# Kernel tuning notes

Measured on AMD Instinct MI355X. Metric: run time of the kernel, lower is better.

Reference implementation:

```python
import jax, jax.numpy as jnp
import numpy as np

HEADS = 8
DIM_HEAD = 64


def setup_inputs() -> dict:
    key = jax.random.key(0)
    ks = jax.random.split(key, 5)
    dim = 512
    dim_inner = HEADS * DIM_HEAD
    return {
        "fmap": jax.random.normal(ks[0], (8, dim, 32, 32), dtype=jnp.float32),
        "gamma": jnp.ones((dim,), dtype=jnp.float32),
        "wq": jax.random.normal(ks[1], (dim_inner, dim), dtype=jnp.float32) * 0.05,
        "wv": jax.random.normal(ks[2], (dim_inner, dim), dtype=jnp.float32) * 0.05,
        "null_kv": jax.random.normal(ks[3], (2, HEADS, DIM_HEAD), dtype=jnp.float32),
        "wo": jax.random.normal(ks[4], (dim, dim_inner), dtype=jnp.float32) * 0.05,
    }


def reference(fmap, gamma, wq, wv, null_kv, wo):
    b, c, H, W = fmap.shape
    h, d = HEADS, DIM_HEAD
    n = H * W
    scale = d ** (-0.5)

    # ChannelRMSNorm: F.normalize over channel dim * sqrt(dim) * gamma
    l2 = jnp.sqrt(jnp.sum(fmap * fmap, axis=1, keepdims=True))
    x = fmap / jnp.maximum(l2, 1e-12) * (c ** 0.5) * gamma[None, :, None, None]

    # 1x1 convs as channel matmuls -> [b, h, n, d]
    def proj(w):
        t = jnp.einsum('bcxy,oc->boxy', x, w)          # [b, h*d, H, W]
        return t.reshape(b, h, d, n).transpose(0, 1, 3, 2)  # [b, h, n, d]

    q = proj(wq)
    v = proj(wv)
    k = q  # dot_product=False -> to_k is None, k = q

    # prepend null kv token
    nk = jnp.broadcast_to(null_kv[0][None, :, None, :], (b, h, 1, d))
    nv = jnp.broadcast_to(null_kv[1][None, :, None, :], (b, h, 1, d))
    k = jnp.concatenate([nk, k], axis=2)  # [b, h, n+1, d]
    v = jnp.concatenate([nv, v], axis=2)

    # negative squared L2 distance score: -(|q|^2 + |k|^2 - 2 q.k)
    q_sq = jnp.sum(q * q, axis=-1)  # [b, h, n]
    k_sq = jnp.sum(k * k, axis=-1)  # [b, h, n+1]
    qk = jnp.einsum('bhid,bhjd->bhij', q, k)
    sim = -(q_sq[..., :, None] + k_sq[..., None, :] - 2.0 * qk) * scale

    attn = jax.nn.softmax(sim, axis=-1)
    out = jnp.einsum('bhij,bhjd->bhid', attn, v)  # [b, h, n, d]

    out = out.transpose(0, 1, 3, 2).reshape(b, h * d, H, W)
    return jnp.einsum('boxy,co->bcxy', out, wo)
```

## Files before the change

kernel.cpp:

```cpp
#include <hip/hip_runtime.h>
#include <hip/hip_bf16.h>

#define DEV static __device__ __forceinline__

typedef __bf16 bf16x8 __attribute__((ext_vector_type(8)));
typedef float f32x4 __attribute__((ext_vector_type(4)));
typedef float f32x16 __attribute__((ext_vector_type(16)));
typedef unsigned u32x4 __attribute__((ext_vector_type(4)));
typedef unsigned short u16x8 __attribute__((ext_vector_type(8)));
typedef unsigned short u16x4 __attribute__((ext_vector_type(4)));

DEV unsigned short f2bf(float f) {
  unsigned u = __builtin_bit_cast(unsigned, f);
  u += 0x7fffu + ((u >> 16) & 1u);
  return (unsigned short)(u >> 16);
}
DEV float bf2f(unsigned short s) {
  return __builtin_bit_cast(float, (unsigned)s << 16);
}
DEV f32x4 mfma16(bf16x8 a, bf16x8 b, f32x4 c) {
  return __builtin_amdgcn_mfma_f32_16x16x32_bf16(a, b, c, 0, 0, 0);
}
DEV f32x16 mfma32(bf16x8 a, bf16x8 b, f32x16 c) {
  return __builtin_amdgcn_mfma_f32_32x32x16_bf16(a, b, c, 0, 0, 0);
}
DEV bf16x8 ld8(const unsigned short* p) {
  return __builtin_bit_cast(bf16x8, *(const u16x8*)p);
}
DEV void gload16(const unsigned short* g, unsigned short* l) {
  auto* g1 = reinterpret_cast<const __attribute__((address_space(1))) unsigned int*>(
      reinterpret_cast<uintptr_t>(g));
  auto* l3 = reinterpret_cast<__attribute__((address_space(3))) unsigned int*>(
      reinterpret_cast<uintptr_t>(l));
  __builtin_amdgcn_global_load_lds(g1, l3, 16, 0, 0);
}

__global__ __launch_bounds__(256) void prep_k(const float* __restrict__ fmap,
                                              const float* __restrict__ gamma,
                                              const float* __restrict__ wq,
                                              const float* __restrict__ wv,
                                              const float* __restrict__ wo,
                                              unsigned short* __restrict__ xt,
                                              unsigned short* __restrict__ wqb,
                                              unsigned short* __restrict__ wvb,
                                              unsigned short* __restrict__ wob) {
  int bid = blockIdx.x, tid = threadIdx.x;
  if (bid >= 256) {
    int t4 = bid - 256;
    int g = t4 >> 5;
    const float* src = (g == 0) ? wq : (g == 1) ? wv : wo;
    unsigned short* dst = (g == 0) ? wqb : (g == 1) ? wvb : wob;
    int base = (t4 & 31) * 1024 + tid;
    const float4* s = (const float4*)src;
#pragma unroll
    for (int i = 0; i < 4; ++i) {
      int idx = base + i * 256;
      float4 a = s[idx * 2], b = s[idx * 2 + 1];
      u16x8 o;
      o[0] = f2bf(a.x); o[1] = f2bf(a.y); o[2] = f2bf(a.z); o[3] = f2bf(a.w);
      o[4] = f2bf(b.x); o[5] = f2bf(b.y); o[6] = f2bf(b.z); o[7] = f2bf(b.w);
      ((u16x8*)dst)[idx] = o;
    }
    return;
  }
  __shared__ float red[8][32];
  __shared__ float rn_l[32];
  __shared__ float gl[512];
  __shared__ float t[64][33];
  int b = bid >> 5, n0 = (bid & 31) * 32;
  gl[tid] = gamma[tid];
  gl[tid + 256] = gamma[tid + 256];
  int n_l = tid & 31, cg = tid >> 5;
  const float* p = fmap + ((size_t)(b * 512 + cg * 64)) * 1024 + n0 + n_l;
  float s = 0.f;
#pragma unroll 16
  for (int i = 0; i < 64; ++i) { float v = p[i * 1024]; s += v * v; }
  red[cg][n_l] = s;
  __syncthreads();
  if (tid < 32) {
    float ts = 0.f;
#pragma unroll
    for (int k = 0; k < 8; ++k) ts += red[k][tid];
    rn_l[tid] = 22.62741699796952f / fmaxf(sqrtf(ts), 1e-12f);
  }
  __syncthreads();
  int nn = tid >> 3, cc = tid & 7;
  for (int c0 = 0; c0 < 512; c0 += 64) {
#pragma unroll
    for (int i = 0; i < 8; ++i)
      t[cg * 8 + i][n_l] = fmap[((size_t)(b * 512 + c0 + cg * 8 + i)) * 1024 + n0 + n_l];
    __syncthreads();
    float sc = rn_l[nn];
    u16x8 o;
#pragma unroll
    for (int e = 0; e < 8; ++e) o[e] = f2bf(t[cc * 8 + e][nn] * sc * gl[c0 + cc * 8 + e]);
    *(u16x8*)(xt + ((size_t)(b * 1024 + n0 + nn)) * 512 + c0 + cc * 8) = o;
    __syncthreads();
  }
}

__global__ __launch_bounds__(256) void gemm_qv_k(const unsigned short* __restrict__ A,
                                                 const unsigned short* __restrict__ wqb,
                                                 const unsigned short* __restrict__ wvb,
                                                 const float* __restrict__ nkv,
                                                 unsigned short* __restrict__ QF,
                                                 unsigned short* __restrict__ VF,
                                                 float* __restrict__ qsqs,
                                                 float* __restrict__ p0g) {
  __shared__ unsigned short a_lds[128 * 64];
  __shared__ unsigned short b_lds[128 * 64];
  const unsigned short* Bt = blockIdx.z ? wvb : wqb;
  int tid = threadIdx.x, lane = tid & 63, wid = tid >> 6;
  int wr = wid >> 1, wc = wid & 1;
  int m0 = blockIdx.y * 128, n0 = blockIdx.x * 128;
  int srow = (lane >> 3);
  int scol = ((lane & 7) ^ ((lane >> 3) & 7)) * 8;
  f32x4 acc[4][4] = {};
  for (int kt = 0; kt < 512; kt += 64) {
#pragma unroll
    for (int i = 0; i < 4; ++i) {
      int il = wid * 4 + i;
      gload16(A + (size_t)(m0 + il * 8 + srow) * 512 + kt + scol, &a_lds[il * 512]);
      gload16(Bt + (size_t)(n0 + il * 8 + srow) * 512 + kt + scol, &b_lds[il * 512]);
    }
    __syncthreads();
#pragma unroll
    for (int ks = 0; ks < 2; ++ks) {
      int c = ks * 4 + (lane >> 4);
      int cs = (c ^ (lane & 7)) * 8;
      bf16x8 af[4], bfr[4];
#pragma unroll
      for (int rt = 0; rt < 4; ++rt)
        af[rt] = ld8(&a_lds[(wr * 64 + rt * 16 + (lane & 15)) * 64 + cs]);
#pragma unroll
      for (int ct = 0; ct < 4; ++ct)
        bfr[ct] = ld8(&b_lds[(wc * 64 + ct * 16 + (lane & 15)) * 64 + cs]);
#pragma unroll
      for (int rt = 0; rt < 4; ++rt)
#pragma unroll
        for (int ct = 0; ct < 4; ++ct)
          acc[rt][ct] = mfma16(af[rt], bfr[ct], acc[rt][ct]);
    }
    __syncthreads();
  }
  if (blockIdx.z == 0) {
    const float COEF = 0.18033688011112042f;
    int head = blockIdx.x * 2 + wc;
    const float* nk = nkv + head * 64;
    float nk_own[4], nks = 0.f;
#pragma unroll
    for (int ct = 0; ct < 4; ++ct) {
      nk_own[ct] = nk[ct * 16 + (lane & 15)];
      nks += nk_own[ct] * nk_own[ct];
    }
    nks += __shfl_xor(nks, 1); nks += __shfl_xor(nks, 2);
    nks += __shfl_xor(nks, 4); nks += __shfl_xor(nks, 8);
#pragma unroll
    for (int rt = 0; rt < 4; ++rt)
#pragma unroll
      for (int r = 0; r < 4; ++r) {
        float qs = 0.f, dot = 0.f;
        unsigned short qr[4];
#pragma unroll
        for (int ct = 0; ct < 4; ++ct) {
          unsigned short us = f2bf(acc[rt][ct][r]);
          qr[ct] = us;
          float v = bf2f(us);
          qs += v * v;
          dot += v * nk_own[ct];
        }
        int n = m0 + wr * 64 + rt * 16 + (lane >> 4) * 4 + r;
        int bb = n >> 10, nl = n & 1023;
        int bh = bb * 8 + head;
        size_t fidx = (size_t)(bh * 32 + (nl >> 5)) * 2048 + (nl & 31) * 16 + (lane & 15);
#pragma unroll
        for (int ct = 0; ct < 4; ++ct) QF[fidx + ct * 512] = qr[ct];
        qs += __shfl_xor(qs, 1); qs += __shfl_xor(qs, 2);
        qs += __shfl_xor(qs, 4); qs += __shfl_xor(qs, 8);
        dot += __shfl_xor(dot, 1); dot += __shfl_xor(dot, 2);
        dot += __shfl_xor(dot, 4); dot += __shfl_xor(dot, 8);
        if ((lane & 15) == 0) {
          qsqs[bh * 1024 + nl] = qs * COEF;
          p0g[bh * 1024 + nl] = __builtin_amdgcn_exp2f((2.f * dot - nks) * COEF);
        }
      }
  } else {
#pragma unroll
    for (int rt = 0; rt < 4; ++rt)
#pragma unroll
      for (int ct = 0; ct < 4; ++ct) {
        int nb = m0 + wr * 64 + rt * 16 + (lane >> 4) * 4;
        int o = n0 + wc * 64 + ct * 16 + (lane & 15);
        int b = nb >> 10, j = nb & 1023;
        int h = o >> 6, d = o & 63;
        int bh = b * 8 + h;
        size_t idx = (size_t)(bh * 32 + (j >> 5)) * 2048 + ((j >> 4) & 1) * 1024 + (d >> 5) * 512 +
                     (d & 31) * 16 + (j & 15);
        u16x4 pk;
#pragma unroll
        for (int r = 0; r < 4; ++r) pk[r] = f2bf(acc[rt][ct][r]);
        *(u16x4*)(VF + idx) = pk;
      }
  }
}

__global__ __launch_bounds__(256) void gemm_o_k(const unsigned short* __restrict__ A,
                                                const unsigned short* __restrict__ Bt,
                                                float* __restrict__ Cp) {
  __shared__ unsigned short a_lds[64 * 64];
  __shared__ unsigned short b_lds[128 * 64];
  int bid = blockIdx.x;
  int y = (bid >> 3) & 7;
  int x = (bid & 7) + ((bid >> 6) << 3);
  int m0 = y * 64, n0 = x * 128;
  int tid = threadIdx.x, lane = tid & 63, wid = tid >> 6;
  int wr = wid >> 1, wc = wid & 1;
  int srow = (lane >> 3);
  int scol = ((lane & 7) ^ ((lane >> 3) & 7)) * 8;
  f32x4 acc[2][4] = {};
  for (int kt = 0; kt < 512; kt += 64) {
#pragma unroll
    for (int i = 0; i < 2; ++i) {
      int il = wid * 2 + i;
      gload16(A + (size_t)(m0 + il * 8 + srow) * 512 + kt + scol, &a_lds[il * 512]);
    }
#pragma unroll
    for (int i = 0; i < 4; ++i) {
      int il = wid * 4 + i;
      gload16(Bt + (size_t)(n0 + il * 8 + srow) * 512 + kt + scol, &b_lds[il * 512]);
    }
    __syncthreads();
#pragma unroll
    for (int ks = 0; ks < 2; ++ks) {
      int c = ks * 4 + (lane >> 4);
      int cs = (c ^ (lane & 7)) * 8;
      bf16x8 af[2], bfr[4];
#pragma unroll
      for (int rt = 0; rt < 2; ++rt)
        af[rt] = ld8(&a_lds[(wr * 32 + rt * 16 + (lane & 15)) * 64 + cs]);
#pragma unroll
      for (int ct = 0; ct < 4; ++ct)
        bfr[ct] = ld8(&b_lds[(wc * 64 + ct * 16 + (lane & 15)) * 64 + cs]);
#pragma unroll
      for (int rt = 0; rt < 2; ++rt)
#pragma unroll
        for (int ct = 0; ct < 4; ++ct)
          acc[rt][ct] = mfma16(af[rt], bfr[ct], acc[rt][ct]);
    }
    __syncthreads();
  }
  int bb = n0 >> 10;
#pragma unroll
  for (int rt = 0; rt < 2; ++rt)
#pragma unroll
    for (int ct = 0; ct < 4; ++ct)
#pragma unroll
      for (int r = 0; r < 4; ++r) {
        int row = m0 + wr * 32 + rt * 16 + (lane >> 4) * 4 + r;
        int col = (n0 & 1023) + wc * 64 + ct * 16 + (lane & 15);
        Cp[((size_t)(bb * 512 + row)) * 1024 + col] = acc[rt][ct][r];
      }
}

__global__ __launch_bounds__(512) void attn_k(const unsigned short* __restrict__ QF,
                                              const unsigned short* __restrict__ VF,
                                              const float* __restrict__ qsqs,
                                              const float* __restrict__ p0g,
                                              const float* __restrict__ nkv,
                                              unsigned short* __restrict__ att) {
  const float C2 = 0.36067376022224085f;
  int bid = blockIdx.x;
  int s0 = bid >> 3;
  int bh = ((bid & 7) << 3) | (s0 & 7);
  int qt = s0 >> 3;
  int b = bh >> 3, h = bh & 7;
  int n0 = qt * 128;
  int tid = threadIdx.x, lane = tid & 63, wid = tid >> 6;
  int wq = wid & 3, jg = wid >> 2;
  int l31 = lane & 31, hi = lane >> 5;

  __shared__ float ob_l[32][4][64];
  __shared__ float dsb[4][32];
  __shared__ float p0_l[128];
  __shared__ float nv_l[64];
  __shared__ float dn_l[4][32];

  if (tid < 128) p0_l[tid] = p0g[bh * 1024 + n0 + tid];
  else if (tid < 192) nv_l[tid - 128] = nkv[512 + h * 64 + (tid - 128)];
  __syncthreads();

  bf16x8 qf[4];
  const unsigned short* qfp = QF + (size_t)(bh * 32 + qt * 4 + wq) * 2048 + l31 * 16 + hi * 8;
#pragma unroll
  for (int ks = 0; ks < 4; ++ks)
    qf[ks] = ld8(qfp + ks * 512);

  f32x16 oacc[2];
#pragma unroll
  for (int dh = 0; dh < 2; ++dh)
#pragma unroll
    for (int r = 0; r < 16; ++r) {
      int row = (r & 3) + 8 * (r >> 2) + 4 * hi;
      oacc[dh][r] = (jg == 0) ? p0_l[wq * 32 + row] * nv_l[dh * 32 + l31] : 0.f;
    }

  f32x4 dsum4 = {0.f, 0.f, 0.f, 0.f};
  const unsigned short* kbase = QF + (size_t)bh * 65536 + l31 * 16 + hi * 8;
  const unsigned short* vbase = VF + (size_t)bh * 65536 + l31 * 16 + hi * 8;
  const float* ksb = qsqs + bh * 1024 + 4 * hi;

  bf16x8 kfA[4], kfB[4], vfA[2][2], vfB[2][2];
  f32x4 ksqA[4], ksqB[4];

#define LOADT(S, JT)                                                        \
  {                                                                         \
    const unsigned short* kp_ = kbase + (JT) * 2048;                        \
    kf##S[0] = ld8(kp_);        kf##S[1] = ld8(kp_ + 512);                  \
    kf##S[2] = ld8(kp_ + 1024); kf##S[3] = ld8(kp_ + 1536);                 \
    const unsigned short* vp_ = vbase + (JT) * 2048;                        \
    vf##S[0][0] = ld8(vp_);        vf##S[0][1] = ld8(vp_ + 1024);           \
    vf##S[1][0] = ld8(vp_ + 512);  vf##S[1][1] = ld8(vp_ + 1536);           \
    const float* kq_ = ksb + (JT) * 32;                                     \
    ksq##S[0] = *(const f32x4*)(kq_);      ksq##S[1] = *(const f32x4*)(kq_ + 8);  \
    ksq##S[2] = *(const f32x4*)(kq_ + 16); ksq##S[3] = *(const f32x4*)(kq_ + 24); \
  }

#define COMPT(S)                                                            \
  {                                                                         \
    f32x16 sacc = {};                                                       \
    __builtin_amdgcn_s_setprio(1);                                          \
    sacc = mfma32(kf##S[0], qf[0], sacc);                                   \
    sacc = mfma32(kf##S[1], qf[1], sacc);                                   \
    sacc = mfma32(kf##S[2], qf[2], sacc);                                   \
    sacc = mfma32(kf##S[3], qf[3], sacc);                                   \
    __builtin_amdgcn_s_setprio(0);                                          \
    float p[16];                                                            \
    _Pragma("unroll")                                                       \
    for (int r = 0; r < 16; ++r) {                                          \
      p[r] = __builtin_amdgcn_exp2f(sacc[r] * C2 - ksq##S[r >> 2][r & 3]);  \
      dsum4[r & 3] += p[r];                                                 \
    }                                                                       \
    unsigned w[4][2];                                                       \
    _Pragma("unroll")                                                       \
    for (int m = 0; m < 4; ++m) {                                           \
      asm("v_cvt_pk_bf16_f32 %0, %1, %2" : "=v"(w[m][0]) : "v"(p[4 * m]), "v"(p[4 * m + 1]));     \
      asm("v_cvt_pk_bf16_f32 %0, %1, %2" : "=v"(w[m][1]) : "v"(p[4 * m + 2]), "v"(p[4 * m + 3])); \
    }                                                                       \
    __builtin_amdgcn_s_setprio(1);                                          \
    _Pragma("unroll")                                                       \
    for (int sj = 0; sj < 2; ++sj) {                                        \
      unsigned a0 = w[2 * sj][0], b0 = w[2 * sj + 1][0];                    \
      unsigned a1 = w[2 * sj][1], b1 = w[2 * sj + 1][1];                    \
      asm("v_permlane32_swap_b32 %0, %1" : "+v"(a0), "+v"(b0));             \
      asm("v_permlane32_swap_b32 %0, %1" : "+v"(a1), "+v"(b1));             \
      u32x4 pw; pw[0] = a0; pw[1] = a1; pw[2] = b0; pw[3] = b1;             \
      bf16x8 pa = __builtin_bit_cast(bf16x8, pw);                           \
      oacc[0] = mfma32(pa, vf##S[0][sj], oacc[0]);                          \
      oacc[1] = mfma32(pa, vf##S[1][sj], oacc[1]);                          \
    }                                                                       \
    __builtin_amdgcn_s_setprio(0);                                          \
  }

  int jb = jg * 16;
  LOADT(A, jb)
#pragma unroll 1
  for (int s = 0; s < 7; ++s) {
    LOADT(B, jb + 2 * s + 1)
    COMPT(A)
    LOADT(A, jb + 2 * s + 2)
    COMPT(B)
  }
  LOADT(B, jb + 15)
  COMPT(A)
  COMPT(B)

  float dsum = (dsum4[0] + dsum4[1]) + (dsum4[2] + dsum4[3]);
  dsum += __shfl_xor(dsum, 32);

  if (jg == 1) {
#pragma unroll
    for (int dh = 0; dh < 2; ++dh)
#pragma unroll
      for (int r = 0; r < 16; ++r)
        ob_l[dh * 16 + r][wq][lane] = oacc[dh][r];
    if (hi == 0) dsb[wq][l31] = dsum;
  }
  __syncthreads();
  if (jg == 0) {
#pragma unroll
    for (int dh = 0; dh < 2; ++dh)
#pragma unroll
      for (int r = 0; r < 16; ++r)
        oacc[dh][r] += ob_l[dh * 16 + r][wq][lane];
    dsum += dsb[wq][l31] + p0_l[wq * 32 + l31];
    float rden = 1.0f / dsum;
    if (hi == 0) dn_l[wq][l31] = rden;
  }
  __syncthreads();

  if (jg == 0) {
#pragma unroll
    for (int dh = 0; dh < 2; ++dh)
#pragma unroll
      for (int r = 0; r < 16; ++r) {
        int row = (r & 3) + 8 * (r >> 2) + 4 * hi;
        float o = oacc[dh][r] * dn_l[wq][row];
        att[((size_t)(b * 1024 + n0 + wq * 32 + row)) * 512 + h * 64 + dh * 32 + l31] = f2bf(o);
      }
  }
}

extern "C" void kernel_launch(void* const* d_in, const int* in_sizes, int n_in,
                              void* d_out, int out_size, void* d_ws, size_t ws_size,
                              hipStream_t stream) {
  const float* fmap = (const float*)d_in[0];
  const float* gamma = (const float*)d_in[1];
  const float* wq = (const float*)d_in[2];
  const float* wv = (const float*)d_in[3];
  const float* nkv = (const float*)d_in[4];
  const float* wo = (const float*)d_in[5];
  float* out = (float*)d_out;

  const size_t M4 = (size_t)8192 * 512;
  unsigned short* x_t = (unsigned short*)d_ws;
  unsigned short* QF  = x_t + M4;
  unsigned short* VF  = QF + M4;
  unsigned short* att = VF + M4;
  unsigned short* wqb = att + M4;
  unsigned short* wvb = wqb + (size_t)512 * 512;
  unsigned short* wob = wvb + (size_t)512 * 512;
  float* qsqs = (float*)(wob + (size_t)512 * 512);
  float* p0g  = qsqs + 65536;

  prep_k<<<352, 256, 0, stream>>>(fmap, gamma, wq, wv, wo, x_t, wqb, wvb, wob);
  gemm_qv_k<<<dim3(4, 64, 2), 256, 0, stream>>>(x_t, wqb, wvb, nkv, QF, VF, qsqs, p0g);
  attn_k<<<512, 512, 0, stream>>>(QF, VF, qsqs, p0g, nkv, att);
  gemm_o_k<<<512, 256, 0, stream>>>(wob, att, out);
}
```

Before: 70.05 us.

## Share A tile between Q and V GEMMs; read fmap once in prep

The Q/V projection GEMM now runs both products in one 512-thread block, so the activation tile is loaded into LDS once and used by four Q waves and four V waves. This removes the separate z-dimension launch and halves activation loads from global memory. The prep kernel keeps the whole 512x32 fmap slab in LDS during the norm pass, so the second global read of fmap and the per-chunk barriers go away. The cost is much higher LDS use (about 67KB in prep, 48KB in the GEMM), half as many GEMM blocks, and lower occupancy.

```diff
diff --git a/kernel.cpp b/kernel.cpp
--- a/kernel.cpp
+++ b/kernel.cpp
@@ -63,18 +63,22 @@
     }
     return;
   }
+  __shared__ float slab[512][33];
   __shared__ float red[8][32];
   __shared__ float rn_l[32];
   __shared__ float gl[512];
-  __shared__ float t[64][33];
   int b = bid >> 5, n0 = (bid & 31) * 32;
   gl[tid] = gamma[tid];
   gl[tid + 256] = gamma[tid + 256];
   int n_l = tid & 31, cg = tid >> 5;
   const float* p = fmap + ((size_t)(b * 512 + cg * 64)) * 1024 + n0 + n_l;
   float s = 0.f;
-#pragma unroll 16
-  for (int i = 0; i < 64; ++i) { float v = p[i * 1024]; s += v * v; }
+#pragma unroll 8
+  for (int i = 0; i < 64; ++i) {
+    float v = p[i * 1024];
+    slab[cg * 64 + i][n_l] = v;
+    s += v * v;
+  }
   red[cg][n_l] = s;
   __syncthreads();
   if (tid < 32) {
@@ -85,21 +89,20 @@
   }
   __syncthreads();
   int nn = tid >> 3, cc = tid & 7;
+  float sc = rn_l[nn];
+#pragma unroll
   for (int c0 = 0; c0 < 512; c0 += 64) {
-#pragma unroll
-    for (int i = 0; i < 8; ++i)
-      t[cg * 8 + i][n_l] = fmap[((size_t)(b * 512 + c0 + cg * 8 + i)) * 1024 + n0 + n_l];
-    __syncthreads();
-    float sc = rn_l[nn];
     u16x8 o;
 #pragma unroll
-    for (int e = 0; e < 8; ++e) o[e] = f2bf(t[cc * 8 + e][nn] * sc * gl[c0 + cc * 8 + e]);
+    for (int e = 0; e < 8; ++e) {
+      int c = c0 + cc * 8 + e;
+      o[e] = f2bf(slab[c][nn] * sc * gl[c]);
+    }
     *(u16x8*)(xt + ((size_t)(b * 1024 + n0 + nn)) * 512 + c0 + cc * 8) = o;
-    __syncthreads();
-  }
-}
-
-__global__ __launch_bounds__(256) void gemm_qv_k(const unsigned short* __restrict__ A,
+  }
+}
+
+__global__ __launch_bounds__(512) void gemm_qv_k(const unsigned short* __restrict__ A,
                                                  const unsigned short* __restrict__ wqb,
                                                  const unsigned short* __restrict__ wvb,
                                                  const float* __restrict__ nkv,
@@ -108,22 +111,26 @@
                                                  float* __restrict__ qsqs,
                                                  float* __restrict__ p0g) {
   __shared__ unsigned short a_lds[128 * 64];
-  __shared__ unsigned short b_lds[128 * 64];
-  const unsigned short* Bt = blockIdx.z ? wvb : wqb;
+  __shared__ unsigned short bq_lds[128 * 64];
+  __shared__ unsigned short bv_lds[128 * 64];
   int tid = threadIdx.x, lane = tid & 63, wid = tid >> 6;
-  int wr = wid >> 1, wc = wid & 1;
+  int isV = wid >> 2, gw = wid & 3;
+  int wr = gw >> 1, wc = gw & 1;
   int m0 = blockIdx.y * 128, n0 = blockIdx.x * 128;
   int srow = (lane >> 3);
   int scol = ((lane & 7) ^ ((lane >> 3) & 7)) * 8;
   f32x4 acc[4][4] = {};
   for (int kt = 0; kt < 512; kt += 64) {
-#pragma unroll
-    for (int i = 0; i < 4; ++i) {
-      int il = wid * 4 + i;
+    int il0 = wid * 2;
+#pragma unroll
+    for (int i = 0; i < 2; ++i) {
+      int il = il0 + i;
       gload16(A + (size_t)(m0 + il * 8 + srow) * 512 + kt + scol, &a_lds[il * 512]);
-      gload16(Bt + (size_t)(n0 + il * 8 + srow) * 512 + kt + scol, &b_lds[il * 512]);
+      gload16(wqb + (size_t)(n0 + il * 8 + srow) * 512 + kt + scol, &bq_lds[il * 512]);
+      gload16(wvb + (size_t)(n0 + il * 8 + srow) * 512 + kt + scol, &bv_lds[il * 512]);
     }
     __syncthreads();
+    const unsigned short* bl = isV ? bv_lds : bq_lds;
 #pragma unroll
     for (int ks = 0; ks < 2; ++ks) {
       int c = ks * 4 + (lane >> 4);
@@ -134,7 +141,7 @@
         af[rt] = ld8(&a_lds[(wr * 64 + rt * 16 + (lane & 15)) * 64 + cs]);
 #pragma unroll
       for (int ct = 0; ct < 4; ++ct)
-        bfr[ct] = ld8(&b_lds[(wc * 64 + ct * 16 + (lane & 15)) * 64 + cs]);
+        bfr[ct] = ld8(&bl[(wc * 64 + ct * 16 + (lane & 15)) * 64 + cs]);
 #pragma unroll
       for (int rt = 0; rt < 4; ++rt)
 #pragma unroll
@@ -143,7 +150,7 @@
     }
     __syncthreads();
   }
-  if (blockIdx.z == 0) {
+  if (!isV) {
     const float COEF = 0.18033688011112042f;
     int head = blockIdx.x * 2 + wc;
     const float* nk = nkv + head * 64;
@@ -433,7 +440,7 @@
   float* p0g  = qsqs + 65536;
 
   prep_k<<<352, 256, 0, stream>>>(fmap, gamma, wq, wv, wo, x_t, wqb, wvb, wob);
-  gemm_qv_k<<<dim3(4, 64, 2), 256, 0, stream>>>(x_t, wqb, wvb, nkv, QF, VF, qsqs, p0g);
+  gemm_qv_k<<<dim3(4, 64), 512, 0, stream>>>(x_t, wqb, wvb, nkv, QF, VF, qsqs, p0g);
   attn_k<<<512, 512, 0, stream>>>(QF, VF, qsqs, p0g, nkv, att);
   gemm_o_k<<<512, 256, 0, stream>>>(wob, att, out);
 }
```

Result: no change. 69.84 us (-0.3%).
